# Kernel tuning notes

Measured on AMD Instinct MI355X. Metric: run time of the kernel, lower is better.

The kernel has to match this reference:

```python
import jax, jax.numpy as jnp
import numpy as np


def _patches(x, k):
    """Replicate F.unfold(x[None,None], kernel_size=k, padding=k//2).
    x: [H, W] -> [k*k, H, W], zero-padded, row-major kernel order (kh, kw)."""
    H, W = x.shape
    p = k // 2
    xp = jnp.pad(x, p)
    return jnp.stack([xp[i:i + H, j:j + W] for i in range(k) for j in range(k)])


def setup_inputs() -> dict:
    key = jax.random.key(0)
    H, W = 1536, 2048
    predict_counting_map = jax.random.uniform(key, (1, 1, H, W), dtype=jnp.float32)
    return {"predict_counting_map": predict_counting_map, "loc_kernel_size": 3, "stride": 4}


def reference(predict_counting_map, loc_kernel_size, stride):
    k = loc_kernel_size
    center = (k * k) // 2
    threshold = 0.5
    m = jax.nn.relu(predict_counting_map[0, 0])            # [H, W] (interpolate scale 1 = identity)
    H, W = m.shape

    patches = _patches(m, k)                               # [k*k, H, W] == unfolded_map
    # local-max mask: argmax over window equals center tap (first-occurrence ties, like torch)
    unfolded_max_mask = (jnp.argmax(patches, axis=0) == center)
    # conv2d with ones kernel == windowed sum of the (zero-padded) patches
    predict_cnt = patches.sum(axis=0)
    predict_filter = (predict_cnt > threshold).astype(jnp.float32) * unfolded_max_mask

    # L1-normalized window weights (F.normalize p=1, eps=1e-12); patches are >= 0 post-relu
    denom = jnp.maximum(jnp.abs(patches).sum(axis=0), 1e-12)
    pred_coord_weight = patches / denom                    # [k*k, H, W]

    coord_h = jnp.broadcast_to(jnp.arange(H, dtype=jnp.float32)[:, None], (H, W))
    coord_w = jnp.broadcast_to(jnp.arange(W, dtype=jnp.float32)[None, :], (H, W))
    pred_coord_h = (_patches(coord_h, k) * pred_coord_weight).sum(axis=0)  # [H, W]
    pred_coord_w = (_patches(coord_w, k) * pred_coord_weight).sum(axis=0)

    # points = stride * coord + 0.5 at pixels where predict_filter is set;
    # returned as fixed-shape maps (filter mask + scaled centroid coords).
    s = jnp.float32(stride)
    out = jnp.stack([predict_filter,
                     s * pred_coord_w + 0.5,
                     s * pred_coord_h + 0.5])              # [3, H, W]
    return out
```

## Files before the change

### kernel.cpp

```cpp
#include <hip/hip_runtime.h>

constexpr int H = 1536;
constexpr int W = 2048;

__global__ __launch_bounds__(256)
void counting_post_kernel(const float* __restrict__ in,
                          const int* __restrict__ stride_p,
                          float* __restrict__ out) {
    const int W4 = W / 4;
    const int tid = blockIdx.x * blockDim.x + threadIdx.x;
    const int r  = tid / W4;
    const int c0 = (tid - r * W4) * 4;
    if (r >= H) return;

    const float s = (float)(*stride_p);

    float v[3][6];
#pragma unroll
    for (int dr = 0; dr < 3; ++dr) {
        const int rr = r + dr - 1;
        if (rr < 0 || rr >= H) {
#pragma unroll
            for (int j = 0; j < 6; ++j) v[dr][j] = 0.f;
        } else {
            const float* row = in + (size_t)rr * W + c0;
            const float4 mid = *reinterpret_cast<const float4*>(row);
            v[dr][1] = fmaxf(mid.x, 0.f);
            v[dr][2] = fmaxf(mid.y, 0.f);
            v[dr][3] = fmaxf(mid.z, 0.f);
            v[dr][4] = fmaxf(mid.w, 0.f);
            v[dr][0] = (c0 > 0)     ? fmaxf(row[-1], 0.f) : 0.f;
            v[dr][5] = (c0 + 4 < W) ? fmaxf(row[4],  0.f) : 0.f;
        }
    }

    float f_o[4], cw_o[4], ch_o[4];
#pragma unroll
    for (int p = 0; p < 4; ++p) {
        const float w00 = v[0][p], w01 = v[0][p+1], w02 = v[0][p+2];
        const float w10 = v[1][p], w11 = v[1][p+1], w12 = v[1][p+2];
        const float w20 = v[2][p], w21 = v[2][p+1], w22 = v[2][p+2];

        const float sum = w00 + w01 + w02 + w10 + w11 + w12 + w20 + w21 + w22;

        const bool mask = (w11 > w00) && (w11 > w01) && (w11 > w02) && (w11 > w10)
                       && (w11 >= w12) && (w11 >= w20) && (w11 >= w21) && (w11 >= w22);
        f_o[p] = (sum > 0.5f && mask) ? 1.f : 0.f;

        const float denom = fmaxf(sum, 1e-12f);
        const float inv   = 1.f / denom;

        const int c = c0 + p;
        const float wh = (float)(r - 1) * (w00 + w01 + w02)
                       + (float)(r    ) * (w10 + w11 + w12)
                       + (float)(r + 1) * (w20 + w21 + w22);
        const float ww = (float)(c - 1) * (w00 + w10 + w20)
                       + (float)(c    ) * (w01 + w11 + w21)
                       + (float)(c + 1) * (w02 + w12 + w22);

        cw_o[p] = s * (ww * inv) + 0.5f;
        ch_o[p] = s * (wh * inv) + 0.5f;
    }

    const size_t base  = (size_t)r * W + c0;
    const size_t plane = (size_t)H * W;
    *reinterpret_cast<float4*>(out + base)             = make_float4(f_o[0],  f_o[1],  f_o[2],  f_o[3]);
    *reinterpret_cast<float4*>(out + plane + base)     = make_float4(cw_o[0], cw_o[1], cw_o[2], cw_o[3]);
    *reinterpret_cast<float4*>(out + 2 * plane + base) = make_float4(ch_o[0], ch_o[1], ch_o[2], ch_o[3]);
}

extern "C" void kernel_launch(void* const* d_in, const int* in_sizes, int n_in,
                              void* d_out, int out_size, void* d_ws, size_t ws_size,
                              hipStream_t stream) {
    const float* in      = (const float*)d_in[0];
    const int*   stride  = (const int*)d_in[2];
    float*       out     = (float*)d_out;

    const int threads = 256;
    const int total   = H * (W / 4);
    const int blocks  = (total + threads - 1) / threads;
    counting_post_kernel<<<blocks, threads, 0, stream>>>(in, stride, out);
}
```

Baseline: 84.16 us.

## Process 8 pixels per thread with separable column sums and nontemporal stores

Each thread now covers 8 pixels and each block one image row, so halo loads are amortized over twice as many outputs. The weighted centroid sums are rewritten algebraically as coordinate times the window sum plus a difference term, built from shared column sums and row differences, which cuts per-pixel arithmetic. Outputs are written with nontemporal stores to avoid cache pollution. The kernel is memory-bound, so the main gain would come from fewer redundant loads and the streaming writes. Fusing the coordinate terms into fmaf could shift rounding slightly.

New measurement: 87.25 us. 1.04x slower.

```diff
diff --git a/kernel.cpp b/kernel.cpp
--- a/kernel.cpp
+++ b/kernel.cpp
@@ -1,83 +1,88 @@
 #include <hip/hip_runtime.h>
 
-constexpr int H = 1536;
-constexpr int W = 2048;
+constexpr int H  = 1536;
+constexpr int W  = 2048;
+constexpr int PX = 8;
+
+typedef float f32x4 __attribute__((ext_vector_type(4)));
 
 __global__ __launch_bounds__(256)
 void counting_post_kernel(const float* __restrict__ in,
                           const int* __restrict__ stride_p,
                           float* __restrict__ out) {
-    const int W4 = W / 4;
-    const int tid = blockIdx.x * blockDim.x + threadIdx.x;
-    const int r  = tid / W4;
-    const int c0 = (tid - r * W4) * 4;
-    if (r >= H) return;
-
+    const int r  = blockIdx.x;
+    const int c0 = threadIdx.x * PX;
     const float s = (float)(*stride_p);
 
-    float v[3][6];
+    float v[3][PX + 2];
 #pragma unroll
     for (int dr = 0; dr < 3; ++dr) {
         const int rr = r + dr - 1;
         if (rr < 0 || rr >= H) {
 #pragma unroll
-            for (int j = 0; j < 6; ++j) v[dr][j] = 0.f;
+            for (int j = 0; j < PX + 2; ++j) v[dr][j] = 0.f;
         } else {
             const float* row = in + (size_t)rr * W + c0;
-            const float4 mid = *reinterpret_cast<const float4*>(row);
-            v[dr][1] = fmaxf(mid.x, 0.f);
-            v[dr][2] = fmaxf(mid.y, 0.f);
-            v[dr][3] = fmaxf(mid.z, 0.f);
-            v[dr][4] = fmaxf(mid.w, 0.f);
-            v[dr][0] = (c0 > 0)     ? fmaxf(row[-1], 0.f) : 0.f;
-            v[dr][5] = (c0 + 4 < W) ? fmaxf(row[4],  0.f) : 0.f;
+            const f32x4 a = *reinterpret_cast<const f32x4*>(row);
+            const f32x4 b = *reinterpret_cast<const f32x4*>(row + 4);
+            v[dr][1] = fmaxf(a.x, 0.f); v[dr][2] = fmaxf(a.y, 0.f);
+            v[dr][3] = fmaxf(a.z, 0.f); v[dr][4] = fmaxf(a.w, 0.f);
+            v[dr][5] = fmaxf(b.x, 0.f); v[dr][6] = fmaxf(b.y, 0.f);
+            v[dr][7] = fmaxf(b.z, 0.f); v[dr][8] = fmaxf(b.w, 0.f);
+            v[dr][0]      = (c0 > 0)      ? fmaxf(row[-1], 0.f) : 0.f;
+            v[dr][PX + 1] = (c0 + PX < W) ? fmaxf(row[PX], 0.f) : 0.f;
         }
     }
 
-    float f_o[4], cw_o[4], ch_o[4];
+    float cs[PX + 2], dv[PX + 2];
 #pragma unroll
-    for (int p = 0; p < 4; ++p) {
-        const float w00 = v[0][p], w01 = v[0][p+1], w02 = v[0][p+2];
-        const float w10 = v[1][p], w11 = v[1][p+1], w12 = v[1][p+2];
-        const float w20 = v[2][p], w21 = v[2][p+1], w22 = v[2][p+2];
+    for (int j = 0; j < PX + 2; ++j) {
+        cs[j] = v[0][j] + v[1][j] + v[2][j];
+        dv[j] = v[2][j] - v[0][j];
+    }
 
-        const float sum = w00 + w01 + w02 + w10 + w11 + w12 + w20 + w21 + w22;
+    float f_o[PX], cw_o[PX], ch_o[PX];
+    const float rf = (float)r;
+#pragma unroll
+    for (int p = 0; p < PX; ++p) {
+        const float sum = cs[p] + cs[p + 1] + cs[p + 2];
+        const float dh  = dv[p] + dv[p + 1] + dv[p + 2];
+        const float dw  = cs[p + 2] - cs[p];
 
-        const bool mask = (w11 > w00) && (w11 > w01) && (w11 > w02) && (w11 > w10)
-                       && (w11 >= w12) && (w11 >= w20) && (w11 >= w21) && (w11 >= w22);
+        const float w11 = v[1][p + 1];
+        const bool mask = (w11 >  v[0][p]) && (w11 >  v[0][p+1]) && (w11 >  v[0][p+2])
+                       && (w11 >  v[1][p])
+                       && (w11 >= v[1][p+2])
+                       && (w11 >= v[2][p]) && (w11 >= v[2][p+1]) && (w11 >= v[2][p+2]);
         f_o[p] = (sum > 0.5f && mask) ? 1.f : 0.f;
 
-        const float denom = fmaxf(sum, 1e-12f);
-        const float inv   = 1.f / denom;
-
-        const int c = c0 + p;
-        const float wh = (float)(r - 1) * (w00 + w01 + w02)
-                       + (float)(r    ) * (w10 + w11 + w12)
-                       + (float)(r + 1) * (w20 + w21 + w22);
-        const float ww = (float)(c - 1) * (w00 + w10 + w20)
-                       + (float)(c    ) * (w01 + w11 + w21)
-                       + (float)(c + 1) * (w02 + w12 + w22);
-
-        cw_o[p] = s * (ww * inv) + 0.5f;
-        ch_o[p] = s * (wh * inv) + 0.5f;
+        const float inv = 1.f / fmaxf(sum, 1e-12f);
+        const float cf  = (float)(c0 + p);
+        const float wh  = fmaf(rf, sum, dh);
+        const float ww  = fmaf(cf, sum, dw);
+        cw_o[p] = fmaf(s, ww * inv, 0.5f);
+        ch_o[p] = fmaf(s, wh * inv, 0.5f);
     }
 
     const size_t base  = (size_t)r * W + c0;
     const size_t plane = (size_t)H * W;
-    *reinterpret_cast<float4*>(out + base)             = make_float4(f_o[0],  f_o[1],  f_o[2],  f_o[3]);
-    *reinterpret_cast<float4*>(out + plane + base)     = make_float4(cw_o[0], cw_o[1], cw_o[2], cw_o[3]);
-    *reinterpret_cast<float4*>(out + 2 * plane + base) = make_float4(ch_o[0], ch_o[1], ch_o[2], ch_o[3]);
+    f32x4* o0 = reinterpret_cast<f32x4*>(out + base);
+    f32x4* o1 = reinterpret_cast<f32x4*>(out + plane + base);
+    f32x4* o2 = reinterpret_cast<f32x4*>(out + 2 * plane + base);
+    __builtin_nontemporal_store((f32x4){f_o[0],  f_o[1],  f_o[2],  f_o[3]},  o0);
+    __builtin_nontemporal_store((f32x4){f_o[4],  f_o[5],  f_o[6],  f_o[7]},  o0 + 1);
+    __builtin_nontemporal_store((f32x4){cw_o[0], cw_o[1], cw_o[2], cw_o[3]}, o1);
+    __builtin_nontemporal_store((f32x4){cw_o[4], cw_o[5], cw_o[6], cw_o[7]}, o1 + 1);
+    __builtin_nontemporal_store((f32x4){ch_o[0], ch_o[1], ch_o[2], ch_o[3]}, o2);
+    __builtin_nontemporal_store((f32x4){ch_o[4], ch_o[5], ch_o[6], ch_o[7]}, o2 + 1);
 }
 
 extern "C" void kernel_launch(void* const* d_in, const int* in_sizes, int n_in,
                               void* d_out, int out_size, void* d_ws, size_t ws_size,
                               hipStream_t stream) {
-    const float* in      = (const float*)d_in[0];
-    const int*   stride  = (const int*)d_in[2];
-    float*       out     = (float*)d_out;
+    const float* in     = (const float*)d_in[0];
+    const int*   stride = (const int*)d_in[2];
+    float*       out    = (float*)d_out;
 
-    const int threads = 256;
-    const int total   = H * (W / 4);
-    const int blocks  = (total + threads - 1) / threads;
-    counting_post_kernel<<<blocks, threads, 0, stream>>>(in, stride, out);
+    counting_post_kernel<<<H, 256, 0, stream>>>(in, stride, out);
 }
```
